# Optimization experiments

Hardware: AMD Instinct MI355X
Metric: run time of the kernel (lower is better)

The kernel has to match this reference:

```python
import jax, jax.numpy as jnp
import numpy as np

H = 8          # nheads
D_OUT = 1024   # tf_out_dim
D_HEAD = D_OUT // H
LN_EPS = 1e-5


def setup_inputs() -> dict:
    key = jax.random.key(0)
    ks = jax.random.split(key, 8)
    n_tok, d_in = 512, 1024
    return {
        "x": jax.random.normal(ks[0], (n_tok, d_in), jnp.float32),
        "c": jax.random.normal(ks[1], (H, n_tok, D_HEAD, D_HEAD), jnp.float32),
        "m_prev": jax.random.normal(ks[2], (H, n_tok, 1), jnp.float32),
        "n_prev": jax.random.normal(ks[3], (H, n_tok, D_HEAD), jnp.float32),
        "Wqkvo": jax.random.normal(ks[4], (d_in, 4 * D_OUT), jnp.float32) * 0.02,
        "bqkvo": jax.random.normal(ks[5], (4 * D_OUT,), jnp.float32) * 0.02,
        "Wuf": jax.random.normal(ks[6], (d_in, 2 * H), jnp.float32) * 0.02,
        "buf": jax.random.normal(ks[7], (2 * H,), jnp.float32) * 0.02,
    }


def reference(x, c, m_prev, n_prev, Wqkvo, bqkvo, Wuf, buf):
    n_tok = x.shape[0]
    scale = jnp.sqrt(jnp.float32(D_HEAD))  # sqrt(tf_out_dim / nheads)

    # projections: 'n (h d) -> h n d'
    qkvo = (x @ Wqkvo + bqkvo).reshape(n_tok, H, 4 * D_HEAD).transpose(1, 0, 2)
    q, k, v, o = jnp.split(qkvo, 4, axis=-1)          # each (H, n, d)
    k = k / scale

    # per-token outer-product update matrix ct = v k^T : (H, n, d, d)
    ct = v[..., :, None] * k[..., None, :]

    uf = (x @ Wuf + buf).reshape(n_tok, H, 2).transpose(1, 0, 2)  # (H, n, 2)
    u, f = uf[..., 0:1], uf[..., 1:2]                  # (H, n, 1)

    # stabilized exp gating (gate='exp', c is not None branch)
    m = jnp.maximum(f + m_prev, u)                     # (H, n, 1)
    ue = jnp.exp(u - m)
    fe = jnp.exp(f + m_prev - m)

    c_new = fe[..., None] * c + ue[..., None] * ct     # (H, n, d, d)
    n_new = fe * n_prev + ue * k                       # (H, n, d)

    # readout (note: original uses ct, not c_new, in the readout einsum)
    h = jnp.einsum('hnkl,hnl->hnk', ct, q)             # (H, n, d)
    nm = jnp.abs(jnp.einsum('hnk,hnk->hn', n_new, q))  # (H, n)
    h = h / jnp.maximum(nm, 1.0)[..., None]
    h = h * jax.nn.sigmoid(o)

    # 'h n d -> n (h d)', residual, LayerNorm over last dim (no affine)
    h = h.transpose(1, 0, 2).reshape(n_tok, D_OUT)
    h = x + h
    mu = jnp.mean(h, axis=-1, keepdims=True)
    var = jnp.var(h, axis=-1, keepdims=True)
    h = (h - mu) / jnp.sqrt(var + LN_EPS)
    return (c_new, h)
```

## Files before the change

kernel.cpp:

```cpp
#include <hip/hip_runtime.h>
#include <hip/hip_bf16.h>
#include <math.h>

#define KSCALE 0.08838834764831845f

typedef __bf16 bf16x8 __attribute__((ext_vector_type(8)));
typedef float  f32x4  __attribute__((ext_vector_type(4)));
typedef unsigned short u16x4 __attribute__((ext_vector_type(4)));
typedef unsigned short u16x8 __attribute__((ext_vector_type(8)));

__device__ inline unsigned short f2bf(float f) {
    unsigned int u = __float_as_uint(f);
    unsigned int r = (u + 0x7FFFu + ((u >> 16) & 1u)) >> 16;
    return (unsigned short)r;
}

__device__ __forceinline__ void gll16(const unsigned short* g, unsigned short* l) {
    __builtin_amdgcn_global_load_lds(
        (const __attribute__((address_space(1))) unsigned int*)g,
        (__attribute__((address_space(3))) unsigned int*)l,
        16, 0, 0);
}

__global__ __launch_bounds__(256) void prep_kernel(const float* __restrict__ x,
                                                   unsigned short* __restrict__ xb,
                                                   const float* __restrict__ W,
                                                   unsigned short* __restrict__ Wt,
                                                   const float* __restrict__ Wuf,
                                                   const float* __restrict__ buf,
                                                   const float* __restrict__ m_prev,
                                                   float* __restrict__ fe_ue) {
    int b = blockIdx.x;
    const int tid = threadIdx.x;
    if (b < 512) {
        int t = b * 256 + tid;
        float4 v = reinterpret_cast<const float4*>(x)[t];
        u16x4 o = { f2bf(v.x), f2bf(v.y), f2bf(v.z), f2bf(v.w) };
        reinterpret_cast<u16x4*>(xb)[t] = o;
    } else if (b < 1536) {
        __shared__ unsigned short tile[64][65];
        int bb = b - 512;
        int k0 = (bb & 15) * 64;
        int n0 = (bb >> 4) * 64;
        int r16 = tid >> 4, c4 = (tid & 15) * 4;
#pragma unroll
        for (int p = 0; p < 4; ++p) {
            int r = p * 16 + r16;
            float4 v = *reinterpret_cast<const float4*>(&W[(size_t)(k0 + r) * 4096 + n0 + c4]);
            tile[r][c4 + 0] = f2bf(v.x);
            tile[r][c4 + 1] = f2bf(v.y);
            tile[r][c4 + 2] = f2bf(v.z);
            tile[r][c4 + 3] = f2bf(v.w);
        }
        __syncthreads();
        int kc = (tid & 7) * 8, r32 = tid >> 3;
#pragma unroll
        for (int p = 0; p < 2; ++p) {
            int rr = p * 32 + r32;
            u16x8 o;
#pragma unroll
            for (int j = 0; j < 8; ++j) o[j] = tile[kc + j][rr];
            *reinterpret_cast<u16x8*>(&Wt[(size_t)(n0 + rr) * 1024 + k0 + kc]) = o;
        }
    } else {
        const int n = b - 1536;
        const int lane = tid & 63, w = tid >> 6;
        const float* xr = x + (size_t)n * 1024;
        float4 p = {0.f, 0.f, 0.f, 0.f};
#pragma unroll
        for (int i = 0; i < 16; ++i) {
            int k = lane + i * 64;
            float xv = xr[k];
            float4 wv = *reinterpret_cast<const float4*>(&Wuf[(size_t)k * 16 + 4 * w]);
            p.x += xv * wv.x; p.y += xv * wv.y; p.z += xv * wv.z; p.w += xv * wv.w;
        }
#pragma unroll
        for (int off = 32; off; off >>= 1) {
            p.x += __shfl_down(p.x, off);
            p.y += __shfl_down(p.y, off);
            p.z += __shfl_down(p.z, off);
            p.w += __shfl_down(p.w, off);
        }
        if (lane == 0) {
#pragma unroll
            for (int t = 0; t < 2; ++t) {
                int h = 2 * w + t;
                float u = (t ? p.z : p.x) + buf[4 * w + 2 * t];
                float f = (t ? p.w : p.y) + buf[4 * w + 2 * t + 1];
                float mp = m_prev[h * 512 + n];
                float m = fmaxf(f + mp, u);
                fe_ue[(h * 512 + n) * 2 + 0] = expf(f + mp - m);
                fe_ue[(h * 512 + n) * 2 + 1] = expf(u - m);
            }
        }
    }
}

__global__ __launch_bounds__(256) void gemm_qkvo(const unsigned short* __restrict__ A,
                                                 const unsigned short* __restrict__ Bt,
                                                 float* __restrict__ Cp) {
    __shared__ __align__(16) unsigned short As[2][64 * 64];
    __shared__ __align__(16) unsigned short Bs[2][64 * 64];
    const int kh = blockIdx.x >> 9;
    const int t9 = blockIdx.x & 511;
    const int bn = t9 & 63;
    const int bm = t9 >> 6;
    const int m0 = bm * 64, n0 = bn * 64;
    const size_t kb0 = (size_t)kh * 512;
    float* C = Cp + (size_t)kh * (512 * 4096);
    const int tid = threadIdx.x;
    const int lane = tid & 63, wave = tid >> 6;
    const int wr = wave >> 1, wc = wave & 1;
    f32x4 acc[2][2] = {};

    const int srow = lane >> 3;
    const int scol = (lane & 7) * 8;

#pragma unroll
    for (int c = 0; c < 2; ++c) {
        int chunk = wave * 2 + c;
        int row = chunk * 8 + srow;
        gll16(A + (size_t)(m0 + row) * 1024 + kb0 + scol, &As[0][chunk * 512]);
        gll16(Bt + (size_t)(n0 + row) * 1024 + kb0 + scol, &Bs[0][chunk * 512]);
    }
    __syncthreads();

    int cur = 0;
    for (int t = 0; t < 8; ++t) {
        if (t < 7) {
            size_t k0 = kb0 + (t + 1) * 64;
#pragma unroll
            for (int c = 0; c < 2; ++c) {
                int chunk = wave * 2 + c;
                int row = chunk * 8 + srow;
                gll16(A + (size_t)(m0 + row) * 1024 + k0 + scol, &As[cur ^ 1][chunk * 512]);
                gll16(Bt + (size_t)(n0 + row) * 1024 + k0 + scol, &Bs[cur ^ 1][chunk * 512]);
            }
        }
        const unsigned short* as = As[cur];
        const unsigned short* bs = Bs[cur];
        const int row = lane & 15;
        const int kof = (lane >> 4) * 8;
#pragma unroll
        for (int kk = 0; kk < 2; ++kk) {
            int kb = kk * 32 + kof;
            bf16x8 a0 = *reinterpret_cast<const bf16x8*>(&as[(wr * 32 + row) * 64 + kb]);
            bf16x8 a1 = *reinterpret_cast<const bf16x8*>(&as[(wr * 32 + 16 + row) * 64 + kb]);
            bf16x8 b0 = *reinterpret_cast<const bf16x8*>(&bs[(wc * 32 + row) * 64 + kb]);
            bf16x8 b1 = *reinterpret_cast<const bf16x8*>(&bs[(wc * 32 + 16 + row) * 64 + kb]);
            acc[0][0] = __builtin_amdgcn_mfma_f32_16x16x32_bf16(a0, b0, acc[0][0], 0, 0, 0);
            acc[0][1] = __builtin_amdgcn_mfma_f32_16x16x32_bf16(a0, b1, acc[0][1], 0, 0, 0);
            acc[1][0] = __builtin_amdgcn_mfma_f32_16x16x32_bf16(a1, b0, acc[1][0], 0, 0, 0);
            acc[1][1] = __builtin_amdgcn_mfma_f32_16x16x32_bf16(a1, b1, acc[1][1], 0, 0, 0);
        }
        __syncthreads();
        cur ^= 1;
    }

    const int cn = lane & 15, cm = (lane >> 4) * 4;
#pragma unroll
    for (int i = 0; i < 2; ++i)
#pragma unroll
        for (int j = 0; j < 2; ++j) {
            int gm = m0 + wr * 32 + i * 16 + cm;
            int gn = n0 + wc * 32 + j * 16 + cn;
#pragma unroll
            for (int v = 0; v < 4; ++v)
                C[(size_t)(gm + v) * 4096 + gn] = acc[i][j][v];
        }
}

__global__ __launch_bounds__(256) void fuse_main(const float* __restrict__ qkvo,
                                                 const float* __restrict__ bias,
                                                 const float* __restrict__ c_in,
                                                 const float* __restrict__ n_prev,
                                                 const float* __restrict__ fe_ue,
                                                 float* __restrict__ c_out,
                                                 float* __restrict__ hst) {
    const int blk = blockIdx.x;
    const int h = blk >> 9, n = blk & 511;
    const int tid = threadIdx.x;
    __shared__ float k_s[128], v_s[128];
    __shared__ float rkq[4], rnq[4];

    const float* baseA = qkvo + (size_t)n * 4096 + h * 512;
    const float* baseB = baseA + (size_t)512 * 4096;
    const float fe = fe_ue[(h * 512 + n) * 2 + 0];
    const float ue = fe_ue[(h * 512 + n) * 2 + 1];

    float kq_p = 0.f, nq_p = 0.f;
    if (tid < 128) {
        float q = baseA[tid] + baseB[tid] + bias[h * 512 + tid];
        float k = (baseA[128 + tid] + baseB[128 + tid] + bias[h * 512 + 128 + tid]) * KSCALE;
        float v = baseA[256 + tid] + baseB[256 + tid] + bias[h * 512 + 256 + tid];
        k_s[tid] = k;
        v_s[tid] = v;
        float nn = fe * n_prev[(size_t)(h * 512 + n) * 128 + tid] + ue * k;
        kq_p = k * q;
        nq_p = nn * q;
    }
#pragma unroll
    for (int off = 32; off; off >>= 1) {
        kq_p += __shfl_down(kq_p, off);
        nq_p += __shfl_down(nq_p, off);
    }
    if ((tid & 63) == 0) { rkq[tid >> 6] = kq_p; rnq[tid >> 6] = nq_p; }
    __syncthreads();
    const float kq = rkq[0] + rkq[1];
    const float nm = fabsf(rnq[0] + rnq[1]);
    const float g = kq / fmaxf(nm, 1.0f);

    const f32x4* cin4 = reinterpret_cast<const f32x4*>(c_in + (size_t)(h * 512 + n) * 16384);
    f32x4* cout4 = reinterpret_cast<f32x4*>(c_out + (size_t)(h * 512 + n) * 16384);
#pragma unroll
    for (int it = 0; it < 16; ++it) {
        int e4 = tid + it * 256;
        int i = e4 >> 5;
        int j4 = (e4 & 31) * 4;
        f32x4 cv = __builtin_nontemporal_load(&cin4[e4]);
        float uv = ue * v_s[i];
        f32x4 o;
        o.x = fe * cv.x + uv * k_s[j4 + 0];
        o.y = fe * cv.y + uv * k_s[j4 + 1];
        o.z = fe * cv.z + uv * k_s[j4 + 2];
        o.w = fe * cv.w + uv * k_s[j4 + 3];
        __builtin_nontemporal_store(o, &cout4[e4]);
    }

    if (tid < 128) {
        float o = baseA[384 + tid] + baseB[384 + tid] + bias[h * 512 + 384 + tid];
        float sig = 1.f / (1.f + expf(-o));
        hst[(size_t)n * 1024 + h * 128 + tid] = v_s[tid] * g * sig;
    }
}

__global__ __launch_bounds__(256) void ln_kernel(const float* __restrict__ x,
                                                 const float* __restrict__ hst,
                                                 float* __restrict__ out) {
    int n = blockIdx.x, tid = threadIdx.x;
    float4 hv = reinterpret_cast<const float4*>(hst + (size_t)n * 1024)[tid];
    float4 xv = reinterpret_cast<const float4*>(x + (size_t)n * 1024)[tid];
    float4 s = { hv.x + xv.x, hv.y + xv.y, hv.z + xv.z, hv.w + xv.w };
    float sum = s.x + s.y + s.z + s.w;
    float sq = s.x * s.x + s.y * s.y + s.z * s.z + s.w * s.w;
#pragma unroll
    for (int off = 32; off; off >>= 1) {
        sum += __shfl_down(sum, off);
        sq += __shfl_down(sq, off);
    }
    __shared__ float rs[4], rq[4];
    if ((tid & 63) == 0) { rs[tid >> 6] = sum; rq[tid >> 6] = sq; }
    __syncthreads();
    sum = rs[0] + rs[1] + rs[2] + rs[3];
    sq = rq[0] + rq[1] + rq[2] + rq[3];
    float mu = sum * (1.f / 1024.f);
    float var = sq * (1.f / 1024.f) - mu * mu;
    float inv = rsqrtf(var + 1e-5f);
    float4 o4 = { (s.x - mu) * inv, (s.y - mu) * inv, (s.z - mu) * inv, (s.w - mu) * inv };
    reinterpret_cast<float4*>(out)[(size_t)n * 256 + tid] = o4;
}

extern "C" void kernel_launch(void* const* d_in, const int* in_sizes, int n_in,
                              void* d_out, int out_size, void* d_ws, size_t ws_size,
                              hipStream_t stream) {
    const float* x      = (const float*)d_in[0];
    const float* c_in   = (const float*)d_in[1];
    const float* m_prev = (const float*)d_in[2];
    const float* n_prev = (const float*)d_in[3];
    const float* Wqkvo  = (const float*)d_in[4];
    const float* bqkvo  = (const float*)d_in[5];
    const float* Wuf    = (const float*)d_in[6];
    const float* buf    = (const float*)d_in[7];
    float* out = (float*)d_out;
    char* ws = (char*)d_ws;

    unsigned short* xb   = (unsigned short*)(ws);
    unsigned short* Wt   = (unsigned short*)(ws + (1u << 20));
    float* qkvo          = (float*)(ws + 9u * (1u << 20));
    float* fe_ue         = (float*)(ws + 25u * (1u << 20));
    float* hst           = (float*)(ws + 25u * (1u << 20) + (1u << 16));

    prep_kernel<<<dim3(2048), dim3(256), 0, stream>>>(x, xb, Wqkvo, Wt, Wuf, buf, m_prev, fe_ue);
    gemm_qkvo  <<<dim3(1024), dim3(256), 0, stream>>>(xb, Wt, qkvo);
    fuse_main  <<<dim3(4096), dim3(256), 0, stream>>>(qkvo, bqkvo, c_in, n_prev, fe_ue, out, hst);
    ln_kernel  <<<dim3(512),  dim3(256), 0, stream>>>(x, hst, out + 67108864ull);
}
```

Before: 129.5 us.

## Split per-token gating/readout+LayerNorm from the c-state streaming kernel

Moves the q/k/v/o assembly, readout and LayerNorm into one per-token kernel that also writes ue*v, k and fe to a small workspace. A separate lean kernel then streams c_in to c_out using those precomputed vectors, so the bandwidth-bound stream has no reductions and only light prologue work. The hst round-trip and the ln_kernel launch are removed. The stream kernel still depends on a preceding small kernel, so the launch count stays the same.

```diff
diff --git a/kernel.cpp b/kernel.cpp
--- a/kernel.cpp
+++ b/kernel.cpp
@@ -13,6 +13,13 @@
     unsigned int u = __float_as_uint(f);
     unsigned int r = (u + 0x7FFFu + ((u >> 16) & 1u)) >> 16;
     return (unsigned short)r;
+}
+
+__device__ __forceinline__ f32x4 LD4(const float* p) {
+    return *reinterpret_cast<const f32x4*>(p);
+}
+__device__ __forceinline__ void ST4(float* p, f32x4 v) {
+    *reinterpret_cast<f32x4*>(p) = v;
 }
 
 __device__ __forceinline__ void gll16(const unsigned short* g, unsigned short* l) {
@@ -170,94 +177,102 @@
         }
 }
 
-__global__ __launch_bounds__(256) void fuse_main(const float* __restrict__ qkvo,
-                                                 const float* __restrict__ bias,
-                                                 const float* __restrict__ c_in,
-                                                 const float* __restrict__ n_prev,
-                                                 const float* __restrict__ fe_ue,
-                                                 float* __restrict__ c_out,
-                                                 float* __restrict__ hst) {
-    const int blk = blockIdx.x;
-    const int h = blk >> 9, n = blk & 511;
+__global__ __launch_bounds__(256) void mid_kernel(const float* __restrict__ qkvo,
+                                                  const float* __restrict__ bias,
+                                                  const float* __restrict__ x,
+                                                  const float* __restrict__ n_prev,
+                                                  const float* __restrict__ fe_ue,
+                                                  float* __restrict__ uvk,
+                                                  float* __restrict__ fe_arr,
+                                                  float* __restrict__ h_out) {
+    const int n = blockIdx.x;
     const int tid = threadIdx.x;
-    __shared__ float k_s[128], v_s[128];
-    __shared__ float rkq[4], rnq[4];
-
-    const float* baseA = qkvo + (size_t)n * 4096 + h * 512;
-    const float* baseB = baseA + (size_t)512 * 4096;
-    const float fe = fe_ue[(h * 512 + n) * 2 + 0];
-    const float ue = fe_ue[(h * 512 + n) * 2 + 1];
-
-    float kq_p = 0.f, nq_p = 0.f;
-    if (tid < 128) {
-        float q = baseA[tid] + baseB[tid] + bias[h * 512 + tid];
-        float k = (baseA[128 + tid] + baseB[128 + tid] + bias[h * 512 + 128 + tid]) * KSCALE;
-        float v = baseA[256 + tid] + baseB[256 + tid] + bias[h * 512 + 256 + tid];
-        k_s[tid] = k;
-        v_s[tid] = v;
-        float nn = fe * n_prev[(size_t)(h * 512 + n) * 128 + tid] + ue * k;
-        kq_p = k * q;
-        nq_p = nn * q;
-    }
-#pragma unroll
-    for (int off = 32; off; off >>= 1) {
-        kq_p += __shfl_down(kq_p, off);
-        nq_p += __shfl_down(nq_p, off);
-    }
-    if ((tid & 63) == 0) { rkq[tid >> 6] = kq_p; rnq[tid >> 6] = nq_p; }
+    const int g = tid >> 5, l = tid & 31;
+    __shared__ float hs_s[1024];
+    __shared__ float red[8];
+
+    const float* bA = qkvo + (size_t)n * 4096 + g * 512;
+    const float* bB = bA + (size_t)512 * 4096;
+    const float* bs = bias + g * 512;
+    const int d4 = l * 4;
+    const int hn = g * 512 + n;
+
+    f32x4 q = LD4(bA + d4)       + LD4(bB + d4)       + LD4(bs + d4);
+    f32x4 k = (LD4(bA + 128 + d4) + LD4(bB + 128 + d4) + LD4(bs + 128 + d4)) * KSCALE;
+    f32x4 v = LD4(bA + 256 + d4) + LD4(bB + 256 + d4) + LD4(bs + 256 + d4);
+    f32x4 o = LD4(bA + 384 + d4) + LD4(bB + 384 + d4) + LD4(bs + 384 + d4);
+    const float fe = fe_ue[hn * 2 + 0];
+    const float ue = fe_ue[hn * 2 + 1];
+    f32x4 np = LD4(n_prev + (size_t)hn * 128 + d4);
+    f32x4 nn = fe * np + ue * k;
+
+    float kq = q[0]*k[0] + q[1]*k[1] + q[2]*k[2] + q[3]*k[3];
+    float nq = q[0]*nn[0] + q[1]*nn[1] + q[2]*nn[2] + q[3]*nn[3];
+#pragma unroll
+    for (int off = 16; off; off >>= 1) {
+        kq += __shfl_down(kq, off, 32);
+        nq += __shfl_down(nq, off, 32);
+    }
+    kq = __shfl(kq, 0, 32);
+    nq = __shfl(nq, 0, 32);
+    const float gs = kq / fmaxf(fabsf(nq), 1.0f);
+
+    ST4(uvk + (size_t)hn * 256 + d4, ue * v);
+    ST4(uvk + (size_t)hn * 256 + 128 + d4, k);
+    if (l == 0) fe_arr[hn] = fe;
+
+#pragma unroll
+    for (int j = 0; j < 4; ++j)
+        hs_s[g * 128 + d4 + j] = v[j] * gs / (1.f + expf(-o[j]));
     __syncthreads();
-    const float kq = rkq[0] + rkq[1];
-    const float nm = fabsf(rnq[0] + rnq[1]);
-    const float g = kq / fmaxf(nm, 1.0f);
-
-    const f32x4* cin4 = reinterpret_cast<const f32x4*>(c_in + (size_t)(h * 512 + n) * 16384);
-    f32x4* cout4 = reinterpret_cast<f32x4*>(c_out + (size_t)(h * 512 + n) * 16384);
-#pragma unroll
-    for (int it = 0; it < 16; ++it) {
-        int e4 = tid + it * 256;
-        int i = e4 >> 5;
-        int j4 = (e4 & 31) * 4;
-        f32x4 cv = __builtin_nontemporal_load(&cin4[e4]);
-        float uv = ue * v_s[i];
-        f32x4 o;
-        o.x = fe * cv.x + uv * k_s[j4 + 0];
-        o.y = fe * cv.y + uv * k_s[j4 + 1];
-        o.z = fe * cv.z + uv * k_s[j4 + 2];
-        o.w = fe * cv.w + uv * k_s[j4 + 3];
-        __builtin_nontemporal_store(o, &cout4[e4]);
-    }
-
-    if (tid < 128) {
-        float o = baseA[384 + tid] + baseB[384 + tid] + bias[h * 512 + 384 + tid];
-        float sig = 1.f / (1.f + expf(-o));
-        hst[(size_t)n * 1024 + h * 128 + tid] = v_s[tid] * g * sig;
-    }
-}
-
-__global__ __launch_bounds__(256) void ln_kernel(const float* __restrict__ x,
-                                                 const float* __restrict__ hst,
-                                                 float* __restrict__ out) {
-    int n = blockIdx.x, tid = threadIdx.x;
-    float4 hv = reinterpret_cast<const float4*>(hst + (size_t)n * 1024)[tid];
-    float4 xv = reinterpret_cast<const float4*>(x + (size_t)n * 1024)[tid];
-    float4 s = { hv.x + xv.x, hv.y + xv.y, hv.z + xv.z, hv.w + xv.w };
-    float sum = s.x + s.y + s.z + s.w;
-    float sq = s.x * s.x + s.y * s.y + s.z * s.z + s.w * s.w;
+
+    f32x4 hv = *reinterpret_cast<const f32x4*>(&hs_s[tid * 4]);
+    f32x4 xv = LD4(x + (size_t)n * 1024 + tid * 4);
+    f32x4 s = hv + xv;
+    float sum = s[0] + s[1] + s[2] + s[3];
+    float sq  = s[0]*s[0] + s[1]*s[1] + s[2]*s[2] + s[3]*s[3];
 #pragma unroll
     for (int off = 32; off; off >>= 1) {
         sum += __shfl_down(sum, off);
-        sq += __shfl_down(sq, off);
-    }
-    __shared__ float rs[4], rq[4];
-    if ((tid & 63) == 0) { rs[tid >> 6] = sum; rq[tid >> 6] = sq; }
+        sq  += __shfl_down(sq, off);
+    }
+    const int wv = tid >> 6;
+    if ((tid & 63) == 0) { red[wv] = sum; red[4 + wv] = sq; }
     __syncthreads();
-    sum = rs[0] + rs[1] + rs[2] + rs[3];
-    sq = rq[0] + rq[1] + rq[2] + rq[3];
+    sum = red[0] + red[1] + red[2] + red[3];
+    sq  = red[4] + red[5] + red[6] + red[7];
     float mu = sum * (1.f / 1024.f);
     float var = sq * (1.f / 1024.f) - mu * mu;
     float inv = rsqrtf(var + 1e-5f);
-    float4 o4 = { (s.x - mu) * inv, (s.y - mu) * inv, (s.z - mu) * inv, (s.w - mu) * inv };
-    reinterpret_cast<float4*>(out)[(size_t)n * 256 + tid] = o4;
+    ST4(h_out + (size_t)n * 1024 + tid * 4, (s - mu) * inv);
+}
+
+__global__ __launch_bounds__(256) void stream_c(const float* __restrict__ c_in,
+                                                const float* __restrict__ uvk,
+                                                const float* __restrict__ fe_arr,
+                                                float* __restrict__ c_out) {
+    const int hn = blockIdx.x;
+    const int tid = threadIdx.x;
+    __shared__ __align__(16) float kv_s[256];
+    if (tid < 64)
+        *reinterpret_cast<f32x4*>(&kv_s[tid * 4]) = LD4(uvk + (size_t)hn * 256 + tid * 4);
+    const float fe = fe_arr[hn];
+    __syncthreads();
+
+    const int j4 = (tid & 31) * 4;
+    const f32x4 kk = *reinterpret_cast<const f32x4*>(&kv_s[128 + j4]);
+    const int i0 = tid >> 5;
+
+    const f32x4* cin4 = reinterpret_cast<const f32x4*>(c_in + (size_t)hn * 16384);
+    f32x4* cout4 = reinterpret_cast<f32x4*>(c_out + (size_t)hn * 16384);
+#pragma unroll
+    for (int it = 0; it < 16; ++it) {
+        int e4 = tid + it * 256;
+        float uvi = kv_s[i0 + it * 8];
+        f32x4 cv = __builtin_nontemporal_load(&cin4[e4]);
+        f32x4 ov = fe * cv + uvi * kk;
+        __builtin_nontemporal_store(ov, &cout4[e4]);
+    }
 }
 
 extern "C" void kernel_launch(void* const* d_in, const int* in_sizes, int n_in,
@@ -278,10 +293,12 @@
     unsigned short* Wt   = (unsigned short*)(ws + (1u << 20));
     float* qkvo          = (float*)(ws + 9u * (1u << 20));
     float* fe_ue         = (float*)(ws + 25u * (1u << 20));
-    float* hst           = (float*)(ws + 25u * (1u << 20) + (1u << 16));
+    float* fe_arr        = (float*)(ws + 25u * (1u << 20) + (1u << 16));
+    float* uvk           = (float*)(ws + 26u * (1u << 20));
 
     prep_kernel<<<dim3(2048), dim3(256), 0, stream>>>(x, xb, Wqkvo, Wt, Wuf, buf, m_prev, fe_ue);
     gemm_qkvo  <<<dim3(1024), dim3(256), 0, stream>>>(xb, Wt, qkvo);
-    fuse_main  <<<dim3(4096), dim3(256), 0, stream>>>(qkvo, bqkvo, c_in, n_prev, fe_ue, out, hst);
-    ln_kernel  <<<dim3(512),  dim3(256), 0, stream>>>(x, hst, out + 67108864ull);
-}
+    mid_kernel <<<dim3(512),  dim3(256), 0, stream>>>(qkvo, bqkvo, x, n_prev, fe_ue,
+                                                      uvk, fe_arr, out + 67108864ull);
+    stream_c   <<<dim3(4096), dim3(256), 0, stream>>>(c_in, uvk, fe_arr, out);
+}
```

New measurement: 127.6 us. No clear change (-1.5%).
